# Optimization experiments

Measured on AMD Instinct MI355X. Metric: run time of the kernel, lower is better.

## Reference

```python
import jax, jax.numpy as jnp
import numpy as np

B, N, K = 8192, 2048, 4  # batch, nodes, neighbors (original: 45, 168, 4)


def _collect_and_transfer(x, adj):
    # x: (B, N), adj: (N, K) int indices of neighbors.
    # Original builds, per node i, a (B, K) block of gathered neighbor values,
    # stacks to (N, B, K), then raw-reshapes (view) to (B, 1, K, N).
    g = jnp.transpose(x[:, adj], (1, 0, 2))   # (N, B, K)
    return g.reshape(x.shape[0], 1, K, adj.shape[0])  # memory reinterpretation, as in .view


def reference(x, label, adj, conv_w, conv_b, lin_w, lin_b):
    a = jnp.concatenate([_collect_and_transfer(x, adj),
                         _collect_and_transfer(label, adj)], axis=1)  # (B, 2, K, N)
    # Conv2d(2 -> 1, kernel=(1,4), stride=(1,4)): (B, 1, K, N//4)
    y = jax.lax.conv_general_dilated(
        a, conv_w, window_strides=(1, 4), padding='VALID',
        dimension_numbers=('NCHW', 'OIHW', 'NCHW'))
    y = jax.nn.relu(y + conv_b[None, :, None, None])
    y = y.reshape(B, N)              # K * (N//4) == N
    return y @ lin_w.T + lin_b       # Linear(N, N)


def setup_inputs() -> dict:
    key = jax.random.key(0)
    k1, k2, k3, k4, k5 = jax.random.split(key, 5)
    return {
        'x': jax.random.normal(k1, (B, N), dtype=jnp.float32),
        'label': jax.random.normal(k2, (B, N), dtype=jnp.float32),
        'adj': jax.random.randint(k3, (N, K), 0, N, dtype=jnp.int32),
        'conv_w': jax.random.normal(k4, (1, 2, 1, 4), dtype=jnp.float32) * 0.1,
        'conv_b': jnp.zeros((1,), dtype=jnp.float32),
        'lin_w': jax.random.normal(k5, (N, N), dtype=jnp.float32) * 0.02,
        'lin_b': jnp.zeros((N,), dtype=jnp.float32),
    }
```

## Files before the change

kernel.cpp:

```cpp
#include <hip/hip_runtime.h>

typedef __bf16 bf16;
typedef bf16 bf16x8 __attribute__((ext_vector_type(8)));
typedef float f32x4 __attribute__((ext_vector_type(4)));
typedef unsigned short ushort;
typedef ushort ushort4v __attribute__((ext_vector_type(4)));

#define BB 8192
#define NN 2048

__device__ __forceinline__ void async16(const void* g, void* l) {
    __builtin_amdgcn_global_load_lds(
        (__attribute__((address_space(1))) void*)(void*)g,
        (__attribute__((address_space(3))) void*)l,
        16, 0, 0);
}

__global__ __launch_bounds__(256) void conv_gather(
    const float* __restrict__ x, const float* __restrict__ label,
    const int* __restrict__ adj, const float* __restrict__ cw,
    const float* __restrict__ cb, bf16* __restrict__ V) {
    __shared__ float4 sxl[NN];
    const int bb0 = blockIdx.x * 2;
    const int t   = threadIdx.x;

    const float4* x0 = (const float4*)(x     + (size_t)bb0 * NN);
    const float4* x1 = (const float4*)(x     + (size_t)(bb0 + 1) * NN);
    const float4* l0 = (const float4*)(label + (size_t)bb0 * NN);
    const float4* l1 = (const float4*)(label + (size_t)(bb0 + 1) * NN);
#pragma unroll
    for (int q = 0; q < 2; ++q) {
        int i = q * 256 + t;
        float4 a = x0[i], b = l0[i], c = x1[i], d = l1[i];
        int n0i = i * 4;
        int sx  = (i >> 1) & 7;
        sxl[(n0i + 0) ^ sx] = make_float4(a.x, b.x, c.x, d.x);
        sxl[(n0i + 1) ^ sx] = make_float4(a.y, b.y, c.y, d.y);
        sxl[(n0i + 2) ^ sx] = make_float4(a.z, b.z, c.z, d.z);
        sxl[(n0i + 3) ^ sx] = make_float4(a.w, b.w, c.w, d.w);
    }
    const float w0 = cw[0], w1 = cw[1], w2 = cw[2], w3 = cw[3];
    const float w4 = cw[4], w5 = cw[5], w6 = cw[6], w7 = cw[7];
    const float bias = cb[0];

    const int4* adj4 = (const int4*)adj;
    int4 a[8];
#pragma unroll
    for (int j = 0; j < 8; ++j) a[j] = adj4[t * 8 + j];

    __syncthreads();

    bf16 o0[8], o1[8];
#pragma unroll
    for (int j = 0; j < 8; ++j) {
        int4 aa = a[j];
        float4 p0 = sxl[aa.x ^ ((aa.x >> 3) & 7)];
        float4 p1 = sxl[aa.y ^ ((aa.y >> 3) & 7)];
        float4 p2 = sxl[aa.z ^ ((aa.z >> 3) & 7)];
        float4 p3 = sxl[aa.w ^ ((aa.w >> 3) & 7)];
        float v0 = bias
                 + w0 * p0.x + w1 * p1.x + w2 * p2.x + w3 * p3.x
                 + w4 * p0.y + w5 * p1.y + w6 * p2.y + w7 * p3.y;
        float v1 = bias
                 + w0 * p0.z + w1 * p1.z + w2 * p2.z + w3 * p3.z
                 + w4 * p0.w + w5 * p1.w + w6 * p2.w + w7 * p3.w;
        o0[j] = (bf16)fmaxf(v0, 0.0f);
        o1[j] = (bf16)fmaxf(v1, 0.0f);
    }
    *(bf16x8*)(V + (size_t)bb0 * NN + t * 8)       = *(const bf16x8*)o0;
    *(bf16x8*)(V + (size_t)(bb0 + 1) * NN + t * 8) = *(const bf16x8*)o1;
}

__global__ __launch_bounds__(256) void transp_cvtw(
    const ushort* __restrict__ V, ushort* __restrict__ Y,
    const float* __restrict__ W, bf16* __restrict__ Wb) {
    const int b = blockIdx.x;
    if (b >= 4096) {
        size_t i = (size_t)(b - 4096) * 256 + threadIdx.x;
        float4 v0 = ((const float4*)W)[i * 2 + 0];
        float4 v1 = ((const float4*)W)[i * 2 + 1];
        bf16x8 o;
        o[0] = (bf16)v0.x; o[1] = (bf16)v0.y; o[2] = (bf16)v0.z; o[3] = (bf16)v0.w;
        o[4] = (bf16)v1.x; o[5] = (bf16)v1.y; o[6] = (bf16)v1.z; o[7] = (bf16)v1.w;
        ((bf16x8*)Wb)[i] = o;
        return;
    }
    __shared__ __attribute__((aligned(16))) ushort tile[64][68];
    const int g0 = (b & 31) * 64;
    const int p0 = (b >> 5) * 64;
    const int c  = threadIdx.x & 15;
    const int r4 = threadIdx.x >> 4;

#pragma unroll
    for (int pass = 0; pass < 4; ++pass) {
        int r = pass * 16 + r4;
        ushort4v v = *(const ushort4v*)(V + (size_t)(p0 + r) * NN + g0 + c * 4);
        *(ushort4v*)&tile[r][c * 4] = v;
    }
    __syncthreads();
    ushort4v rv[4];
#pragma unroll
    for (int j = 0; j < 4; ++j)
        rv[j] = *(const ushort4v*)&tile[c * 4 + j][r4 * 4];
#pragma unroll
    for (int q = 0; q < 4; ++q) {
        ushort4v o;
        o.x = rv[0][q]; o.y = rv[1][q]; o.z = rv[2][q]; o.w = rv[3][q];
        *(ushort4v*)(Y + (size_t)(g0 + r4 * 4 + q) * BB + p0 + c * 4) = o;
    }
}

__global__ __launch_bounds__(512, 2) void gemm_bt(
    const bf16* __restrict__ A, const bf16* __restrict__ W,
    const float* __restrict__ bias, float* __restrict__ out) {
    __shared__ __attribute__((aligned(16))) bf16 sA[2][16384];
    __shared__ __attribute__((aligned(16))) bf16 sB[2][16384];

    const int t    = threadIdx.x;
    const int lane = t & 63;
    const int wv   = t >> 6;
    const int wm   = wv & 1;
    const int wn   = wv >> 1;
    const int l16  = lane & 15;
    const int l4   = lane >> 4;

    const int xcd = blockIdx.x & 7;
    const int loc = blockIdx.x >> 3;
    const int bx  = xcd * 4 + (loc >> 3);
    const int by  = loc & 7;
    const int m0  = bx * 256;
    const int n0  = by * 256;

    const int r8  = t >> 3;
    const int c8  = ((t & 7) ^ (r8 & 7)) * 8;
    const int dst = t * 8;

    const int sw    = l16 & 7;
    const int aOff0 = (wm * 128 + l16) * 64 + ((l4    ) ^ sw) * 8;
    const int aOff1 = (wm * 128 + l16) * 64 + ((l4 + 4) ^ sw) * 8;
    const int bOff0 = (wn * 64  + l16) * 64 + ((l4    ) ^ sw) * 8;
    const int bOff1 = (wn * 64  + l16) * 64 + ((l4 + 4) ^ sw) * 8;

    f32x4  acc[8][4] = {};
    bf16x8 aR[4][2], bR[4][2];

#define GBAR()  asm volatile("s_barrier" ::: "memory")
#define LGKM0() do { asm volatile("s_waitcnt lgkmcnt(0)" ::: "memory"); \
                     __builtin_amdgcn_sched_barrier(0); } while (0)
#define VMW6()  asm volatile("s_waitcnt vmcnt(6)" ::: "memory")
#define VMW0()  asm volatile("s_waitcnt vmcnt(0)" ::: "memory")

#define STG(G, rb, kt, lp) do {                                           \
        const bf16* _s = (G) + (size_t)((rb) + r8) * 2048 + (kt) + c8;    \
        async16(_s, (lp) + dst);                                          \
        async16(_s + (size_t)64 * 2048, (lp) + 4096 + dst);               \
    } while (0)

#define LDA(sp, mh) do {                                                  \
        const bf16* _p = (sp) + (mh) * 4096;                              \
        aR[0][0] = *(const bf16x8*)(_p + aOff0);                          \
        aR[0][1] = *(const bf16x8*)(_p + aOff1);                          \
        aR[1][0] = *(const bf16x8*)(_p + 1024 + aOff0);                   \
        aR[1][1] = *(const bf16x8*)(_p + 1024 + aOff1);                   \
        aR[2][0] = *(const bf16x8*)(_p + 2048 + aOff0);                   \
        aR[2][1] = *(const bf16x8*)(_p + 2048 + aOff1);                   \
        aR[3][0] = *(const bf16x8*)(_p + 3072 + aOff0);                   \
        aR[3][1] = *(const bf16x8*)(_p + 3072 + aOff1);                   \
    } while (0)

#define LDB(sp, nh) do {                                                  \
        const bf16* _p = (sp) + (nh) * 2048;                              \
        bR[(nh)*2+0][0] = *(const bf16x8*)(_p + bOff0);                   \
        bR[(nh)*2+0][1] = *(const bf16x8*)(_p + bOff1);                   \
        bR[(nh)*2+1][0] = *(const bf16x8*)(_p + 1024 + bOff0);            \
        bR[(nh)*2+1][1] = *(const bf16x8*)(_p + 1024 + bOff1);            \
    } while (0)

#define MM(mh, nh) do {                                                   \
        __builtin_amdgcn_s_setprio(1);                                    \
        _Pragma("unroll")                                                 \
        for (int _ks = 0; _ks < 2; ++_ks)                                 \
            _Pragma("unroll")                                             \
            for (int _mf = 0; _mf < 4; ++_mf)                             \
                _Pragma("unroll")                                         \
                for (int _nf = 0; _nf < 2; ++_nf)                         \
                    acc[(mh)*4+_mf][(nh)*2+_nf] =                         \
                        __builtin_amdgcn_mfma_f32_16x16x32_bf16(          \
                            aR[_mf][_ks], bR[(nh)*2+_nf][_ks],            \
                            acc[(mh)*4+_mf][(nh)*2+_nf], 0, 0, 0);        \
        __builtin_amdgcn_s_setprio(0);                                    \
    } while (0)

    bf16* const sA0 = &sA[0][0]; bf16* const sA1 = &sA[1][0];
    bf16* const sB0 = &sB[0][0]; bf16* const sB1 = &sB[1][0];

    STG(A, m0,       0,  sA0);
    STG(A, m0 + 128, 0,  sA0 + 8192);
    STG(W, n0,       0,  sB0);
    STG(W, n0 + 128, 0,  sB0 + 8192);
    STG(W, n0,       64, sB1);
    STG(W, n0 + 128, 64, sB1 + 8192);
    STG(A, m0,       64, sA1);
    VMW6();
    GBAR();

    for (int i = 0; i < 15; ++i) {
        const int kb = i * 128;
        LDA(sA0, 0); LDB(sB0, 0);
        STG(A, m0 + 128, kb + 64, sA1 + 8192);
        GBAR(); LGKM0();
        MM(0, 0);
        GBAR();
        LDB(sB0, 1);
        GBAR(); LGKM0();
        MM(0, 1);
        GBAR();
        LDA(sA0, 1);
        STG(W, n0, kb + 128, sB0);
        GBAR(); LGKM0();
        MM(1, 0);
        GBAR();
        STG(W, n0 + 128, kb + 128, sB0 + 8192);
        STG(A, m0,       kb + 128, sA0);
        GBAR(); LGKM0();
        MM(1, 1);
        VMW6();
        GBAR();
        LDA(sA1, 0); LDB(sB1, 0);
        STG(A, m0 + 128, kb + 128, sA0 + 8192);
        GBAR(); LGKM0();
        MM(0, 0);
        GBAR();
        LDB(sB1, 1);
        GBAR(); LGKM0();
        MM(0, 1);
        GBAR();
        LDA(sA1, 1);
        STG(W, n0, kb + 192, sB1);
        GBAR(); LGKM0();
        MM(1, 0);
        GBAR();
        STG(W, n0 + 128, kb + 192, sB1 + 8192);
        STG(A, m0,       kb + 192, sA1);
        GBAR(); LGKM0();
        MM(1, 1);
        VMW6();
        GBAR();
    }

    LDA(sA0, 0); LDB(sB0, 0);
    STG(A, m0 + 128, 1984, sA1 + 8192);
    GBAR(); LGKM0(); MM(0, 0); GBAR();
    LDB(sB0, 1);
    GBAR(); LGKM0(); MM(0, 1); GBAR();
    LDA(sA0, 1);
    GBAR(); LGKM0(); MM(1, 0); GBAR();
    GBAR(); LGKM0(); MM(1, 1);
    VMW0();
    GBAR();
    LDA(sA1, 0); LDB(sB1, 0);
    GBAR(); LGKM0(); MM(0, 0); GBAR();
    LDB(sB1, 1);
    GBAR(); LGKM0(); MM(0, 1); GBAR();
    LDA(sA1, 1);
    GBAR(); LGKM0(); MM(1, 0); GBAR();
    GBAR(); LGKM0(); MM(1, 1);

#pragma unroll
    for (int nf = 0; nf < 4; ++nf) {
        const int col = n0 + wn * 64 + nf * 16 + l16;
        const float bc = bias[col];
#pragma unroll
        for (int mf = 0; mf < 8; ++mf) {
            const size_t row = (size_t)(m0 + wm * 128 + mf * 16 + l4 * 4);
#pragma unroll
            for (int rr = 0; rr < 4; ++rr)
                out[(row + rr) * 2048 + col] = acc[mf][nf][rr] + bc;
        }
    }
#undef STG
#undef LDA
#undef LDB
#undef MM
#undef GBAR
#undef LGKM0
#undef VMW6
#undef VMW0
}

extern "C" void kernel_launch(void* const* d_in, const int* in_sizes, int n_in,
                              void* d_out, int out_size, void* d_ws, size_t ws_size,
                              hipStream_t stream) {
    (void)in_sizes; (void)n_in; (void)out_size; (void)ws_size;
    const float* x     = (const float*)d_in[0];
    const float* label = (const float*)d_in[1];
    const int*   adj   = (const int*)d_in[2];
    const float* cw    = (const float*)d_in[3];
    const float* cb    = (const float*)d_in[4];
    const float* lw    = (const float*)d_in[5];
    const float* lb    = (const float*)d_in[6];
    float* out = (float*)d_out;

    bf16* V  = (bf16*)d_out;
    bf16* Y2 = (bf16*)d_ws;
    bf16* Wb = (bf16*)((char*)d_ws + (size_t)2048 * 8192 * 2);

    conv_gather<<<BB / 2, 256, 0, stream>>>(x, label, adj, cw, cb, V);
    transp_cvtw<<<6144, 256, 0, stream>>>((const ushort*)V, (ushort*)Y2,
                                          lw, Wb);
    gemm_bt<<<dim3(256), 512, 0, stream>>>(Y2, Wb, lb, out);
}
```

Baseline: 269.3 us.

## Process four rows per conv block, split GEMM LDS waits, stage epilogue through LDS

The conv_gather kernel now handles four batch rows per block and keeps the gathered inputs in LDS as packed bf16, so each neighbor fetch returns eight values and the block count halves. The GEMM main loop replaces its full lgkmcnt(0) waits and extra barriers with partial waits, so the first half of the MFMAs can start while the remaining LDS fragment loads are still in flight. The epilogue writes accumulators into LDS and reads them back as row-contiguous 16-byte vectors for coalesced global stores, where before it did scattered scalar stores. The costs are rounding the conv inputs to bf16 before the weighted sum, which reduces accuracy, and fewer barriers, which raises the risk of LDS race hazards.

```diff
diff --git a/kernel.cpp b/kernel.cpp
--- a/kernel.cpp
+++ b/kernel.cpp
@@ -20,24 +20,39 @@
     const float* __restrict__ x, const float* __restrict__ label,
     const int* __restrict__ adj, const float* __restrict__ cw,
     const float* __restrict__ cb, bf16* __restrict__ V) {
-    __shared__ float4 sxl[NN];
-    const int bb0 = blockIdx.x * 2;
+    __shared__ bf16x8 sxl[NN];
+    const int bb0 = blockIdx.x * 4;
     const int t   = threadIdx.x;
 
-    const float4* x0 = (const float4*)(x     + (size_t)bb0 * NN);
+    const float4* x0 = (const float4*)(x     + (size_t)(bb0 + 0) * NN);
     const float4* x1 = (const float4*)(x     + (size_t)(bb0 + 1) * NN);
-    const float4* l0 = (const float4*)(label + (size_t)bb0 * NN);
+    const float4* x2 = (const float4*)(x     + (size_t)(bb0 + 2) * NN);
+    const float4* x3 = (const float4*)(x     + (size_t)(bb0 + 3) * NN);
+    const float4* l0 = (const float4*)(label + (size_t)(bb0 + 0) * NN);
     const float4* l1 = (const float4*)(label + (size_t)(bb0 + 1) * NN);
+    const float4* l2 = (const float4*)(label + (size_t)(bb0 + 2) * NN);
+    const float4* l3 = (const float4*)(label + (size_t)(bb0 + 3) * NN);
+
 #pragma unroll
     for (int q = 0; q < 2; ++q) {
         int i = q * 256 + t;
-        float4 a = x0[i], b = l0[i], c = x1[i], d = l1[i];
+        float4 xa = x0[i], xb = x1[i], xc = x2[i], xd = x3[i];
+        float4 la = l0[i], lb2 = l1[i], lc = l2[i], ld2 = l3[i];
         int n0i = i * 4;
         int sx  = (i >> 1) & 7;
-        sxl[(n0i + 0) ^ sx] = make_float4(a.x, b.x, c.x, d.x);
-        sxl[(n0i + 1) ^ sx] = make_float4(a.y, b.y, c.y, d.y);
-        sxl[(n0i + 2) ^ sx] = make_float4(a.z, b.z, c.z, d.z);
-        sxl[(n0i + 3) ^ sx] = make_float4(a.w, b.w, c.w, d.w);
+        bf16x8 e;
+        e[0]=(bf16)xa.x; e[1]=(bf16)la.x;  e[2]=(bf16)xb.x; e[3]=(bf16)lb2.x;
+        e[4]=(bf16)xc.x; e[5]=(bf16)lc.x;  e[6]=(bf16)xd.x; e[7]=(bf16)ld2.x;
+        sxl[(n0i + 0) ^ sx] = e;
+        e[0]=(bf16)xa.y; e[1]=(bf16)la.y;  e[2]=(bf16)xb.y; e[3]=(bf16)lb2.y;
+        e[4]=(bf16)xc.y; e[5]=(bf16)lc.y;  e[6]=(bf16)xd.y; e[7]=(bf16)ld2.y;
+        sxl[(n0i + 1) ^ sx] = e;
+        e[0]=(bf16)xa.z; e[1]=(bf16)la.z;  e[2]=(bf16)xb.z; e[3]=(bf16)lb2.z;
+        e[4]=(bf16)xc.z; e[5]=(bf16)lc.z;  e[6]=(bf16)xd.z; e[7]=(bf16)ld2.z;
+        sxl[(n0i + 2) ^ sx] = e;
+        e[0]=(bf16)xa.w; e[1]=(bf16)la.w;  e[2]=(bf16)xb.w; e[3]=(bf16)lb2.w;
+        e[4]=(bf16)xc.w; e[5]=(bf16)lc.w;  e[6]=(bf16)xd.w; e[7]=(bf16)ld2.w;
+        sxl[(n0i + 3) ^ sx] = e;
     }
     const float w0 = cw[0], w1 = cw[1], w2 = cw[2], w3 = cw[3];
     const float w4 = cw[4], w5 = cw[5], w6 = cw[6], w7 = cw[7];
@@ -50,25 +65,35 @@
 
     __syncthreads();
 
-    bf16 o0[8], o1[8];
+    bf16 o0[8], o1[8], o2[8], o3[8];
 #pragma unroll
     for (int j = 0; j < 8; ++j) {
         int4 aa = a[j];
-        float4 p0 = sxl[aa.x ^ ((aa.x >> 3) & 7)];
-        float4 p1 = sxl[aa.y ^ ((aa.y >> 3) & 7)];
-        float4 p2 = sxl[aa.z ^ ((aa.z >> 3) & 7)];
-        float4 p3 = sxl[aa.w ^ ((aa.w >> 3) & 7)];
+        bf16x8 p0 = sxl[aa.x ^ ((aa.x >> 3) & 7)];
+        bf16x8 p1 = sxl[aa.y ^ ((aa.y >> 3) & 7)];
+        bf16x8 p2 = sxl[aa.z ^ ((aa.z >> 3) & 7)];
+        bf16x8 p3 = sxl[aa.w ^ ((aa.w >> 3) & 7)];
         float v0 = bias
-                 + w0 * p0.x + w1 * p1.x + w2 * p2.x + w3 * p3.x
-                 + w4 * p0.y + w5 * p1.y + w6 * p2.y + w7 * p3.y;
+                 + w0*(float)p0[0] + w1*(float)p1[0] + w2*(float)p2[0] + w3*(float)p3[0]
+                 + w4*(float)p0[1] + w5*(float)p1[1] + w6*(float)p2[1] + w7*(float)p3[1];
         float v1 = bias
-                 + w0 * p0.z + w1 * p1.z + w2 * p2.z + w3 * p3.z
-                 + w4 * p0.w + w5 * p1.w + w6 * p2.w + w7 * p3.w;
+                 + w0*(float)p0[2] + w1*(float)p1[2] + w2*(float)p2[2] + w3*(float)p3[2]
+                 + w4*(float)p0[3] + w5*(float)p1[3] + w6*(float)p2[3] + w7*(float)p3[3];
+        float v2 = bias
+                 + w0*(float)p0[4] + w1*(float)p1[4] + w2*(float)p2[4] + w3*(float)p3[4]
+                 + w4*(float)p0[5] + w5*(float)p1[5] + w6*(float)p2[5] + w7*(float)p3[5];
+        float v3 = bias
+                 + w0*(float)p0[6] + w1*(float)p1[6] + w2*(float)p2[6] + w3*(float)p3[6]
+                 + w4*(float)p0[7] + w5*(float)p1[7] + w6*(float)p2[7] + w7*(float)p3[7];
         o0[j] = (bf16)fmaxf(v0, 0.0f);
         o1[j] = (bf16)fmaxf(v1, 0.0f);
-    }
-    *(bf16x8*)(V + (size_t)bb0 * NN + t * 8)       = *(const bf16x8*)o0;
+        o2[j] = (bf16)fmaxf(v2, 0.0f);
+        o3[j] = (bf16)fmaxf(v3, 0.0f);
+    }
+    *(bf16x8*)(V + (size_t)(bb0 + 0) * NN + t * 8) = *(const bf16x8*)o0;
     *(bf16x8*)(V + (size_t)(bb0 + 1) * NN + t * 8) = *(const bf16x8*)o1;
+    *(bf16x8*)(V + (size_t)(bb0 + 2) * NN + t * 8) = *(const bf16x8*)o2;
+    *(bf16x8*)(V + (size_t)(bb0 + 3) * NN + t * 8) = *(const bf16x8*)o3;
 }
 
 __global__ __launch_bounds__(256) void transp_cvtw(
@@ -144,11 +169,14 @@
     f32x4  acc[8][4] = {};
     bf16x8 aR[4][2], bR[4][2];
 
-#define GBAR()  asm volatile("s_barrier" ::: "memory")
-#define LGKM0() do { asm volatile("s_waitcnt lgkmcnt(0)" ::: "memory"); \
-                     __builtin_amdgcn_sched_barrier(0); } while (0)
-#define VMW6()  asm volatile("s_waitcnt vmcnt(6)" ::: "memory")
-#define VMW0()  asm volatile("s_waitcnt vmcnt(0)" ::: "memory")
+#define GBAR()   asm volatile("s_barrier" ::: "memory")
+#define LGKM(N)  do { asm volatile("s_waitcnt lgkmcnt(" #N ")" ::: "memory"); \
+                      __builtin_amdgcn_sched_barrier(0); } while (0)
+#define LGKMP(N) do { __builtin_amdgcn_sched_barrier(0);                      \
+                      asm volatile("s_waitcnt lgkmcnt(" #N ")" ::: "memory"); \
+                      __builtin_amdgcn_sched_barrier(0); } while (0)
+#define VMW6()   asm volatile("s_waitcnt vmcnt(6)" ::: "memory")
+#define VMW0()   asm volatile("s_waitcnt vmcnt(0)" ::: "memory")
 
 #define STG(G, rb, kt, lp) do {                                           \
         const bf16* _s = (G) + (size_t)((rb) + r8) * 2048 + (kt) + c8;    \
@@ -156,40 +184,44 @@
         async16(_s + (size_t)64 * 2048, (lp) + 4096 + dst);               \
     } while (0)
 
-#define LDA(sp, mh) do {                                                  \
-        const bf16* _p = (sp) + (mh) * 4096;                              \
-        aR[0][0] = *(const bf16x8*)(_p + aOff0);                          \
-        aR[0][1] = *(const bf16x8*)(_p + aOff1);                          \
-        aR[1][0] = *(const bf16x8*)(_p + 1024 + aOff0);                   \
-        aR[1][1] = *(const bf16x8*)(_p + 1024 + aOff1);                   \
-        aR[2][0] = *(const bf16x8*)(_p + 2048 + aOff0);                   \
-        aR[2][1] = *(const bf16x8*)(_p + 2048 + aOff1);                   \
-        aR[3][0] = *(const bf16x8*)(_p + 3072 + aOff0);                   \
-        aR[3][1] = *(const bf16x8*)(_p + 3072 + aOff1);                   \
+#define LDA2(sp, mh, g) do {                                              \
+        const bf16* _p = (sp) + (mh) * 4096 + (g) * 2048;                 \
+        aR[(g)*2+0][0] = *(const bf16x8*)(_p + aOff0);                    \
+        aR[(g)*2+0][1] = *(const bf16x8*)(_p + aOff1);                    \
+        aR[(g)*2+1][0] = *(const bf16x8*)(_p + 1024 + aOff0);             \
+        aR[(g)*2+1][1] = *(const bf16x8*)(_p + 1024 + aOff1);             \
     } while (0)
 
-#define LDB(sp, nh) do {                                                  \
-        const bf16* _p = (sp) + (nh) * 2048;                              \
-        bR[(nh)*2+0][0] = *(const bf16x8*)(_p + bOff0);                   \
-        bR[(nh)*2+0][1] = *(const bf16x8*)(_p + bOff1);                   \
-        bR[(nh)*2+1][0] = *(const bf16x8*)(_p + 1024 + bOff0);            \
-        bR[(nh)*2+1][1] = *(const bf16x8*)(_p + 1024 + bOff1);            \
+#define LDB1(sp, nfA) do {                                                \
+        const bf16* _p = (sp) + ((nfA) >> 1) * 2048 + ((nfA) & 1) * 1024; \
+        bR[nfA][0] = *(const bf16x8*)(_p + bOff0);                        \
+        bR[nfA][1] = *(const bf16x8*)(_p + bOff1);                        \
     } while (0)
 
-#define MM(mh, nh) do {                                                   \
-        __builtin_amdgcn_s_setprio(1);                                    \
+#define MM8_MF(mh, nh, h)                                                 \
+    _Pragma("unroll")                                                     \
+    for (int _ks = 0; _ks < 2; ++_ks)                                     \
         _Pragma("unroll")                                                 \
-        for (int _ks = 0; _ks < 2; ++_ks)                                 \
+        for (int _mf = (h)*2; _mf < (h)*2+2; ++_mf)                       \
             _Pragma("unroll")                                             \
-            for (int _mf = 0; _mf < 4; ++_mf)                             \
-                _Pragma("unroll")                                         \
-                for (int _nf = 0; _nf < 2; ++_nf)                         \
-                    acc[(mh)*4+_mf][(nh)*2+_nf] =                         \
-                        __builtin_amdgcn_mfma_f32_16x16x32_bf16(          \
-                            aR[_mf][_ks], bR[(nh)*2+_nf][_ks],            \
-                            acc[(mh)*4+_mf][(nh)*2+_nf], 0, 0, 0);        \
-        __builtin_amdgcn_s_setprio(0);                                    \
-    } while (0)
+            for (int _nf = 0; _nf < 2; ++_nf)                             \
+                acc[(mh)*4+_mf][(nh)*2+_nf] =                             \
+                    __builtin_amdgcn_mfma_f32_16x16x32_bf16(              \
+                        aR[_mf][_ks], bR[(nh)*2+_nf][_ks],                \
+                        acc[(mh)*4+_mf][(nh)*2+_nf], 0, 0, 0)
+
+#define MM8_NF(mh, nfA)                                                   \
+    _Pragma("unroll")                                                     \
+    for (int _ks = 0; _ks < 2; ++_ks)                                     \
+        _Pragma("unroll")                                                 \
+        for (int _mf = 0; _mf < 4; ++_mf)                                 \
+            acc[(mh)*4+_mf][nfA] =                                        \
+                __builtin_amdgcn_mfma_f32_16x16x32_bf16(                  \
+                    aR[_mf][_ks], bR[nfA][_ks],                           \
+                    acc[(mh)*4+_mf][nfA], 0, 0, 0)
+
+#define PRIO1() __builtin_amdgcn_s_setprio(1)
+#define PRIO0() __builtin_amdgcn_s_setprio(0)
 
     bf16* const sA0 = &sA[0][0]; bf16* const sA1 = &sA[1][0];
     bf16* const sB0 = &sB[0][0]; bf16* const sB1 = &sB[1][0];
@@ -206,86 +238,129 @@
 
     for (int i = 0; i < 15; ++i) {
         const int kb = i * 128;
-        LDA(sA0, 0); LDB(sB0, 0);
+        LDB1(sB0, 0); LDB1(sB0, 1); LDA2(sA0, 0, 0);
+        LDA2(sA0, 0, 1);
         STG(A, m0 + 128, kb + 64, sA1 + 8192);
-        GBAR(); LGKM0();
-        MM(0, 0);
-        GBAR();
-        LDB(sB0, 1);
-        GBAR(); LGKM0();
-        MM(0, 1);
-        GBAR();
-        LDA(sA0, 1);
+        LGKM(4);  PRIO1(); MM8_MF(0, 0, 0);
+        LGKMP(0);          MM8_MF(0, 0, 1); PRIO0();
+        GBAR();
+        LDB1(sB0, 2);
+        LDB1(sB0, 3);
+        LGKM(2);  PRIO1(); MM8_NF(0, 2);
+        LGKMP(0);          MM8_NF(0, 3); PRIO0();
+        GBAR();
+        LDA2(sA0, 1, 0);
+        LDA2(sA0, 1, 1);
         STG(W, n0, kb + 128, sB0);
-        GBAR(); LGKM0();
-        MM(1, 0);
+        LGKM(4);  PRIO1(); MM8_MF(1, 0, 0);
+        LGKMP(0);          MM8_MF(1, 0, 1); PRIO0();
         GBAR();
         STG(W, n0 + 128, kb + 128, sB0 + 8192);
         STG(A, m0,       kb + 128, sA0);
-        GBAR(); LGKM0();
-        MM(1, 1);
+        PRIO1(); MM8_NF(1, 2); MM8_NF(1, 3); PRIO0();
         VMW6();
         GBAR();
-        LDA(sA1, 0); LDB(sB1, 0);
+        LDB1(sB1, 0); LDB1(sB1, 1); LDA2(sA1, 0, 0);
+        LDA2(sA1, 0, 1);
         STG(A, m0 + 128, kb + 128, sA0 + 8192);
-        GBAR(); LGKM0();
-        MM(0, 0);
-        GBAR();
-        LDB(sB1, 1);
-        GBAR(); LGKM0();
-        MM(0, 1);
-        GBAR();
-        LDA(sA1, 1);
+        LGKM(4);  PRIO1(); MM8_MF(0, 0, 0);
+        LGKMP(0);          MM8_MF(0, 0, 1); PRIO0();
+        GBAR();
+        LDB1(sB1, 2);
+        LDB1(sB1, 3);
+        LGKM(2);  PRIO1(); MM8_NF(0, 2);
+        LGKMP(0);          MM8_NF(0, 3); PRIO0();
+        GBAR();
+        LDA2(sA1, 1, 0);
+        LDA2(sA1, 1, 1);
         STG(W, n0, kb + 192, sB1);
-        GBAR(); LGKM0();
-        MM(1, 0);
+        LGKM(4);  PRIO1(); MM8_MF(1, 0, 0);
+        LGKMP(0);          MM8_MF(1, 0, 1); PRIO0();
         GBAR();
         STG(W, n0 + 128, kb + 192, sB1 + 8192);
         STG(A, m0,       kb + 192, sA1);
-        GBAR(); LGKM0();
-        MM(1, 1);
+        PRIO1(); MM8_NF(1, 2); MM8_NF(1, 3); PRIO0();
         VMW6();
         GBAR();
     }
 
-    LDA(sA0, 0); LDB(sB0, 0);
+    LDB1(sB0, 0); LDB1(sB0, 1); LDA2(sA0, 0, 0);
+    LDA2(sA0, 0, 1);
     STG(A, m0 + 128, 1984, sA1 + 8192);
-    GBAR(); LGKM0(); MM(0, 0); GBAR();
-    LDB(sB0, 1);
-    GBAR(); LGKM0(); MM(0, 1); GBAR();
-    LDA(sA0, 1);
-    GBAR(); LGKM0(); MM(1, 0); GBAR();
-    GBAR(); LGKM0(); MM(1, 1);
+    LGKM(4);  PRIO1(); MM8_MF(0, 0, 0);
+    LGKMP(0);          MM8_MF(0, 0, 1); PRIO0();
+    GBAR();
+    LDB1(sB0, 2); LDB1(sB0, 3);
+    LGKM(2);  PRIO1(); MM8_NF(0, 2);
+    LGKMP(0);          MM8_NF(0, 3); PRIO0();
+    GBAR();
+    LDA2(sA0, 1, 0); LDA2(sA0, 1, 1);
+    LGKM(4);  PRIO1(); MM8_MF(1, 0, 0);
+    LGKMP(0);          MM8_MF(1, 0, 1); PRIO0();
+    GBAR();
+    PRIO1(); MM8_NF(1, 2); MM8_NF(1, 3); PRIO0();
     VMW0();
     GBAR();
-    LDA(sA1, 0); LDB(sB1, 0);
-    GBAR(); LGKM0(); MM(0, 0); GBAR();
-    LDB(sB1, 1);
-    GBAR(); LGKM0(); MM(0, 1); GBAR();
-    LDA(sA1, 1);
-    GBAR(); LGKM0(); MM(1, 0); GBAR();
-    GBAR(); LGKM0(); MM(1, 1);
-
-#pragma unroll
-    for (int nf = 0; nf < 4; ++nf) {
-        const int col = n0 + wn * 64 + nf * 16 + l16;
-        const float bc = bias[col];
+    LDB1(sB1, 0); LDB1(sB1, 1); LDA2(sA1, 0, 0);
+    LDA2(sA1, 0, 1);
+    LGKM(4);  PRIO1(); MM8_MF(0, 0, 0);
+    LGKMP(0);          MM8_MF(0, 0, 1); PRIO0();
+    GBAR();
+    LDB1(sB1, 2); LDB1(sB1, 3);
+    LGKM(2);  PRIO1(); MM8_NF(0, 2);
+    LGKMP(0);          MM8_NF(0, 3); PRIO0();
+    GBAR();
+    LDA2(sA1, 1, 0); LDA2(sA1, 1, 1);
+    LGKM(4);  PRIO1(); MM8_MF(1, 0, 0);
+    LGKMP(0);          MM8_MF(1, 0, 1); PRIO0();
+    GBAR();
+    PRIO1(); MM8_NF(1, 2); MM8_NF(1, 3); PRIO0();
+
+    GBAR();
+
+    {
+        float* ep = (float*)&sA[0][0] + wv * (16 * 68);
+        const int cb0 = n0 + wn * 64;
+        float bc[4];
+#pragma unroll
+        for (int nf = 0; nf < 4; ++nf) bc[nf] = bias[cb0 + nf * 16 + l16];
+        const int rw = lane >> 2;
+        const int cg = lane & 3;
 #pragma unroll
         for (int mf = 0; mf < 8; ++mf) {
-            const size_t row = (size_t)(m0 + wm * 128 + mf * 16 + l4 * 4);
-#pragma unroll
-            for (int rr = 0; rr < 4; ++rr)
-                out[(row + rr) * 2048 + col] = acc[mf][nf][rr] + bc;
+#pragma unroll
+            for (int nf = 0; nf < 4; ++nf)
+#pragma unroll
+                for (int rr = 0; rr < 4; ++rr)
+                    ep[(l4 * 4 + rr) * 68 + nf * 16 + l16] =
+                        acc[mf][nf][rr] + bc[nf];
+            asm volatile("s_waitcnt lgkmcnt(0)" ::: "memory");
+            const size_t rowb = (size_t)(m0 + wm * 128 + mf * 16 + rw);
+            float* op = out + rowb * 2048 + cb0 + cg * 16;
+            const float* rp = ep + rw * 68 + cg * 16;
+            f32x4 v0 = *(const f32x4*)(rp + 0);
+            f32x4 v1 = *(const f32x4*)(rp + 4);
+            f32x4 v2 = *(const f32x4*)(rp + 8);
+            f32x4 v3 = *(const f32x4*)(rp + 12);
+            asm volatile("s_waitcnt lgkmcnt(0)" ::: "memory");
+            *(f32x4*)(op + 0)  = v0;
+            *(f32x4*)(op + 4)  = v1;
+            *(f32x4*)(op + 8)  = v2;
+            *(f32x4*)(op + 12) = v3;
         }
     }
 #undef STG
-#undef LDA
-#undef LDB
-#undef MM
+#undef LDA2
+#undef LDB1
+#undef MM8_MF
+#undef MM8_NF
 #undef GBAR
-#undef LGKM0
+#undef LGKM
+#undef LGKMP
 #undef VMW6
 #undef VMW0
+#undef PRIO1
+#undef PRIO0
 }
 
 extern "C" void kernel_launch(void* const* d_in, const int* in_sizes, int n_in,
@@ -305,7 +380,7 @@
     bf16* Y2 = (bf16*)d_ws;
     bf16* Wb = (bf16*)((char*)d_ws + (size_t)2048 * 8192 * 2);
 
-    conv_gather<<<BB / 2, 256, 0, stream>>>(x, label, adj, cw, cb, V);
+    conv_gather<<<BB / 4, 256, 0, stream>>>(x, label, adj, cw, cb, V);
     transp_cvtw<<<6144, 256, 0, stream>>>((const ushort*)V, (ushort*)Y2,
                                           lw, Wb);
     gemm_bt<<<dim3(256), 512, 0, stream>>>(Y2, Wb, lb, out);
```

Measured after the change: 273.9 us. About the same (+1.7%).
